# Kernel tuning notes

Measured on AMD Instinct MI355X. Metric: run time of the kernel, lower is better.

Reference implementation:

```python
import jax, jax.numpy as jnp
import numpy as np

N, L, D, H = 2, 2048, 1024, 16
Dh = D // H          # 64
HIST = 2048          # history_len
SCALE = D ** 0.5     # note: module scales by sqrt(model_dim), not sqrt(head_dim)


def setup_inputs() -> dict:
    key = jax.random.key(0)
    ks = jax.random.split(key, 10)
    f = lambda k, s, sc=1.0: jax.random.normal(k, s, dtype=jnp.float32) * sc
    i = jnp.arange(L)
    causal = i[None, :] > i[:, None]            # mask future
    old = i[None, :] <= i[:, None] - HIST       # mask beyond history window
    mask = causal | old                          # True = masked, (L, L)
    return {
        "values": f(ks[0], (N, L, D)),
        "keys": f(ks[1], (N, L, D)),
        "query": f(ks[2], (N, L, D)),
        "origin_values": f(ks[3], (N, L, D)),
        "origin_keys": f(ks[4], (N, L, D)),
        "Wv": f(ks[5], (Dh, Dh), 0.1),
        "Wk": f(ks[6], (Dh, Dh), 0.1),
        "Wq": f(ks[7], (Dh, Dh), 0.1),
        "fc_w": f(ks[8], (D, D), 0.03),
        "fc_b": jnp.zeros((D,), dtype=jnp.float32),
        "mask": mask,
    }


def reference(values, keys, query, origin_values, origin_keys, Wv, Wk, Wq, fc_w, fc_b, mask):
    # forward(..., ref_sample=True): mfpca_attention path.
    # origin_keys/values are projected exactly as the prior ref_sample=False call stored them.
    split = lambda x: x.reshape(N, L, H, Dh)
    v = split(values) @ Wv.T        # (N, L, H, Dh)  torch Linear: x @ W^T, no bias
    k = split(keys) @ Wk.T
    q = split(query) @ Wq.T
    ov = split(origin_values) @ Wv.T
    ok = split(origin_keys) @ Wk.T

    energy = jnp.einsum('nqhd,nkhd->nhqk', q, ok)       # (N, H, L, L)
    samp_energy = jnp.einsum('nlhd,nlhd->nhl', q, k)    # (N, H, L)
    eye = jnp.eye(L, dtype=bool)
    # energy.diagonal().copy_(samp_energy)
    energy = jnp.where(eye, samp_energy[:, :, None, :], energy)
    energy = jnp.where(mask, jnp.float32(-1e20), energy)
    scores = jax.nn.softmax(energy / SCALE, axis=-1)
    diag_scores = jnp.diagonal(scores, axis1=2, axis2=3)    # (N, H, L)
    scores_nodiag = jnp.where(eye, 0.0, scores)
    # NOTE: original einsum output is indexed by l (not q) -- reproduced faithfully.
    origin_attention = jnp.einsum('nhql,nlhd->nlhd', scores_nodiag, ov)
    samp_attention = jnp.einsum('nhl,nlhd->nlhd', diag_scores, v)
    attention = (samp_attention + origin_attention).reshape(N, L, D)
    return attention @ fc_w.T + fc_b
```

## Files before the change

kernel.cpp:

```cpp
#include <hip/hip_runtime.h>

#define NB 2
#define LL 2048
#define DD 1024
#define HH 16
#define NHH (NB*HH)
#define LT (LL/64)
#define KT16 (LL/16)
#define CEXP 0.0450842200277801f

typedef __bf16 bf16x8 __attribute__((ext_vector_type(8)));
typedef unsigned short u16x8 __attribute__((ext_vector_type(8)));
typedef float f32x4 __attribute__((ext_vector_type(4)));

#define MFMA16 __builtin_amdgcn_mfma_f32_16x16x32_bf16
#define EXP2 __builtin_amdgcn_exp2f
#define LOG2 __builtin_amdgcn_logf

__device__ __forceinline__ unsigned short f2bf(float f) {
    unsigned u = __float_as_uint(f);
    return (unsigned short)((u + 0x7fffu + ((u >> 16) & 1u)) >> 16);
}
__device__ __forceinline__ float bf2f(unsigned short u) {
    return __uint_as_float(((unsigned)u) << 16);
}
__device__ __forceinline__ bf16x8 ldfrag(const unsigned short* p) {
    return *reinterpret_cast<const bf16x8*>(p);
}
__device__ __forceinline__ bf16x8 cvt8v(float4 a, float4 b) {
    u16x8 u;
    u[0]=f2bf(a.x); u[1]=f2bf(a.y); u[2]=f2bf(a.z); u[3]=f2bf(a.w);
    u[4]=f2bf(b.x); u[5]=f2bf(b.y); u[6]=f2bf(b.z); u[7]=f2bf(b.w);
    return __builtin_bit_cast(bf16x8, u);
}
__device__ __forceinline__ ushort4 pack4(f32x4 d, float sc) {
    ushort4 o;
    o.x = f2bf(d[0]*sc); o.y = f2bf(d[1]*sc); o.z = f2bf(d[2]*sc); o.w = f2bf(d[3]*sc);
    return o;
}
__device__ __forceinline__ void gload16(const unsigned short* g, unsigned short* l) {
    __builtin_amdgcn_global_load_lds(
        (const __attribute__((address_space(1))) unsigned int*)g,
        (__attribute__((address_space(3))) unsigned int*)l, 16, 0, 0);
}

__global__ __launch_bounds__(256) void prep_kernel(
    const float* __restrict__ Wk, const float* __restrict__ Wq,
    const float* __restrict__ Wv, unsigned short* __restrict__ wfrag)
{
    const int t = threadIdx.x;
    const int s = blockIdx.x * 256 + t;
    const int m = s >> 9;
    const int rem = s & 511;
    const int f = rem >> 6;
    const int lane = rem & 63;
    const int n16 = lane & 15, quad = lane >> 4;
    const int mt = f >> 1, half = f & 1;
    const float* W = (m == 0) ? Wk : (m == 1) ? Wq : Wv;
    const float* p = W + (mt*16 + n16)*64 + quad*8 + half*32;
    float4 a = *reinterpret_cast<const float4*>(p);
    float4 b = *reinterpret_cast<const float4*>(p + 4);
    *reinterpret_cast<bf16x8*>(wfrag + (size_t)s * 8) = cvt8v(a, b);
}

__global__ __launch_bounds__(256) void proj_kernel(
    const float* __restrict__ values, const float* __restrict__ keys,
    const float* __restrict__ query,  const float* __restrict__ ovals,
    const float* __restrict__ okeys,  const unsigned short* __restrict__ wfrag,
    const float* __restrict__ fc_w,   unsigned short* __restrict__ fcwb,
    unsigned short* __restrict__ qb, unsigned short* __restrict__ okb,
    unsigned short* __restrict__ vb, unsigned short* __restrict__ ovb,
    float* __restrict__ ediag)
{
    const int t = threadIdx.x;
    if (blockIdx.z == 2) {
        const int id = blockIdx.y * 64 + blockIdx.x;
        const int idx = id * 1024 + t * 4;
        float4 wv = *reinterpret_cast<const float4*>(fc_w + idx);
        ushort4 o;
        o.x = f2bf(wv.x); o.y = f2bf(wv.y); o.z = f2bf(wv.z); o.w = f2bf(wv.w);
        *reinterpret_cast<ushort4*>(fcwb + idx) = o;
        return;
    }
    const int w = t >> 6;
    const int lane = t & 63;
    const int n16 = lane & 15;
    const int quad = lane >> 4;
    const int h = blockIdx.y;
    const int row = blockIdx.x * 64 + w * 16 + n16;
    const int nn = row >> 11;
    const int ll = row & 2047;
    const size_t xoff  = (size_t)row * DD + h * 64 + quad * 8;
    const size_t qbase = (((size_t)(nn * HH + h)) * LL + ll) * 64;
    const size_t vbase = (size_t)row * DD + h * 64;

    if (blockIdx.z == 0) {
        const float4* kp = reinterpret_cast<const float4*>(keys  + xoff);
        const float4* qp = reinterpret_cast<const float4*>(query + xoff);
        const float4* op = reinterpret_cast<const float4*>(okeys + xoff);
        float4 k0 = kp[0], k1 = kp[1], k2 = kp[8], k3 = kp[9];
        float4 q0 = qp[0], q1 = qp[1], q2 = qp[8], q3 = qp[9];
        float4 o0 = op[0], o1 = op[1], o2 = op[8], o3 = op[9];
        bf16x8 wk[8], wq[8];
#pragma unroll
        for (int f = 0; f < 8; ++f) {
            wk[f] = ldfrag(wfrag + (size_t)(f * 64 + lane) * 8);
            wq[f] = ldfrag(wfrag + (size_t)((8 + f) * 64 + lane) * 8);
        }
        bf16x8 xk0 = cvt8v(k0, k1), xk1 = cvt8v(k2, k3);
        bf16x8 xq0 = cvt8v(q0, q1), xq1 = cvt8v(q2, q3);
        bf16x8 xo0 = cvt8v(o0, o1), xo1 = cvt8v(o2, o3);
        f32x4 ka[4], qa[4];
#pragma unroll
        for (int mt = 0; mt < 4; ++mt) {
            f32x4 d = {0.f,0.f,0.f,0.f};
            d = MFMA16(wk[mt*2], xk0, d, 0,0,0);
            ka[mt] = MFMA16(wk[mt*2+1], xk1, d, 0,0,0);
        }
#pragma unroll
        for (int mt = 0; mt < 4; ++mt) {
            f32x4 d = {0.f,0.f,0.f,0.f};
            d = MFMA16(wq[mt*2], xq0, d, 0,0,0);
            qa[mt] = MFMA16(wq[mt*2+1], xq1, d, 0,0,0);
            *reinterpret_cast<ushort4*>(qb + qbase + mt*16 + quad*4) = pack4(qa[mt], CEXP);
        }
#pragma unroll
        for (int mt = 0; mt < 4; ++mt) {
            f32x4 d = {0.f,0.f,0.f,0.f};
            d = MFMA16(wk[mt*2], xo0, d, 0,0,0);
            d = MFMA16(wk[mt*2+1], xo1, d, 0,0,0);
            *reinterpret_cast<ushort4*>(okb + qbase + mt*16 + quad*4) = pack4(d, 1.0f);
        }
        float p = 0.f;
#pragma unroll
        for (int mt = 0; mt < 4; ++mt)
            p += qa[mt][0]*ka[mt][0] + qa[mt][1]*ka[mt][1]
               + qa[mt][2]*ka[mt][2] + qa[mt][3]*ka[mt][3];
        p += __shfl_xor(p, 16);
        p += __shfl_xor(p, 32);
        if (lane < 16)
            ediag[((size_t)(nn * HH + h)) * LL + ll] = p;
    } else {
        const float4* vp = reinterpret_cast<const float4*>(values + xoff);
        const float4* op = reinterpret_cast<const float4*>(ovals  + xoff);
        float4 v0 = vp[0], v1 = vp[1], v2 = vp[8], v3 = vp[9];
        float4 o0 = op[0], o1 = op[1], o2 = op[8], o3 = op[9];
        bf16x8 wv[8];
#pragma unroll
        for (int f = 0; f < 8; ++f)
            wv[f] = ldfrag(wfrag + (size_t)((16 + f) * 64 + lane) * 8);
        bf16x8 xv0 = cvt8v(v0, v1), xv1 = cvt8v(v2, v3);
        bf16x8 xo0 = cvt8v(o0, o1), xo1 = cvt8v(o2, o3);
#pragma unroll
        for (int mt = 0; mt < 4; ++mt) {
            f32x4 d = {0.f,0.f,0.f,0.f};
            d = MFMA16(wv[mt*2], xv0, d, 0,0,0);
            d = MFMA16(wv[mt*2+1], xv1, d, 0,0,0);
            *reinterpret_cast<ushort4*>(vb + vbase + mt*16 + quad*4) = pack4(d, 1.0f);
        }
#pragma unroll
        for (int mt = 0; mt < 4; ++mt) {
            f32x4 d = {0.f,0.f,0.f,0.f};
            d = MFMA16(wv[mt*2], xo0, d, 0,0,0);
            d = MFMA16(wv[mt*2+1], xo1, d, 0,0,0);
            *reinterpret_cast<ushort4*>(ovb + vbase + mt*16 + quad*4) = pack4(d, 1.0f);
        }
    }
}

__global__ __launch_bounds__(256) void zrow_part(
    const unsigned short* __restrict__ qb, const unsigned short* __restrict__ okb,
    float* __restrict__ Zbuf)
{
    __shared__ unsigned short slds[2][64 * 64];

    const int bid = blockIdx.x;
    const int nh = bid & 31;
    const int qt = 31 - (bid >> 5);
    const int t = threadIdx.x;
    const int w = t >> 6;
    const int lane = t & 63;
    const int n = lane & 15;
    const int quad = lane >> 4;
    const size_t base = (size_t)nh * (LL * 64);
    const size_t nhL = (size_t)nh * LL;

    const unsigned short* bp = qb + base + (size_t)(qt*64 + w*16 + n) * 64 + quad * 8;
    const bf16x8 bq0 = ldfrag(bp);
    const bf16x8 bq1 = ldfrag(bp + 32);

    const int srow = t >> 3;
    const int schunk = (t & 7) ^ (srow & 7);
    const int soff = srow * 64 + schunk * 8;
    const int nst = qt + 1;

    {
        const unsigned short* s0 = okb + base + soff;
        gload16(s0, &slds[0][t * 8]);
        gload16(s0 + 32 * 64, &slds[0][2048 + t * 8]);
    }
    __syncthreads();

    const int rs0 = (quad ^ (n & 7)) * 8;
    const int rs1 = ((quad + 4) ^ (n & 7)) * 8;

    float zacc = 0.f;
    int buf = 0;
    for (int si = 0; si < nst; ++si) {
        if (si + 1 < nst) {
            const unsigned short* s0 = okb + base + (size_t)((si + 1) * 64) * 64 + soff;
            gload16(s0, &slds[buf ^ 1][t * 8]);
            gload16(s0 + 32 * 64, &slds[buf ^ 1][2048 + t * 8]);
        }
        const unsigned short* S = &slds[buf][0];
        const bool dstrip = (si == qt);
#pragma unroll
        for (int sub = 0; sub < 4; ++sub) {
            if (dstrip && sub > w) continue;
            const int row = sub * 16 + n;
            const bf16x8 a0 = ldfrag(S + row * 64 + rs0);
            const bf16x8 a1 = ldfrag(S + row * 64 + rs1);
            f32x4 d = {0.f, 0.f, 0.f, 0.f};
            d = MFMA16(a0, bq0, d, 0, 0, 0);
            d = MFMA16(a1, bq1, d, 0, 0, 0);
            if (dstrip && sub == w) {
#pragma unroll
                for (int r = 0; r < 4; ++r)
                    if (quad * 4 + r < n) zacc += EXP2(d[r]);
            } else {
#pragma unroll
                for (int r = 0; r < 4; ++r) zacc += EXP2(d[r]);
            }
        }
        __syncthreads();
        buf ^= 1;
    }

    zacc += __shfl_down(zacc, 32);
    zacc += __shfl_down(zacc, 16);
    if (lane < 16)
        Zbuf[nhL + qt * 64 + w * 16 + lane] = zacc;
}

__global__ __launch_bounds__(256) void colsum_part(
    const unsigned short* __restrict__ qb, const unsigned short* __restrict__ okb,
    const float* __restrict__ Zbuf, const float* __restrict__ ediag,
    float* __restrict__ colsum)
{
    __shared__ unsigned short slds[2][64 * 64];
    __shared__ __align__(16) float izlds[2][64];

    const int bid = blockIdx.x;
    const int nh = bid & 31;
    const int lt = bid >> 5;
    const int t = threadIdx.x;
    const int w = t >> 6;
    const int lane = t & 63;
    const int n = lane & 15;
    const int quad = lane >> 4;
    const size_t base = (size_t)nh * (LL * 64);
    const size_t nhL = (size_t)nh * LL;

    const unsigned short* bp = okb + base + (size_t)(lt*64 + w*16 + n) * 64 + quad * 8;
    const bf16x8 bl0 = ldfrag(bp);
    const bf16x8 bl1 = ldfrag(bp + 32);

    const int srow = t >> 3;
    const int schunk = (t & 7) ^ (srow & 7);
    const int soff = srow * 64 + schunk * 8;
    const int nst = 32 - lt;
    const int q00 = lt * 64;

    {
        const unsigned short* s0 = qb + base + (size_t)q00 * 64 + soff;
        gload16(s0, &slds[0][t * 8]);
        gload16(s0 + 32 * 64, &slds[0][2048 + t * 8]);
        if (t < 64) {
            const float z = Zbuf[nhL + q00 + t];
            const float e = ediag[nhL + q00 + t];
            izlds[0][t] = -LOG2(z + EXP2(e * CEXP));
        }
    }
    __syncthreads();

    const int rs0 = (quad ^ (n & 7)) * 8;
    const int rs1 = ((quad + 4) ^ (n & 7)) * 8;

    float cacc = 0.f;
    int buf = 0;
    for (int si = 0; si < nst; ++si) {
        if (si + 1 < nst) {
            const int qn = q00 + (si + 1) * 64;
            const unsigned short* s0 = qb + base + (size_t)qn * 64 + soff;
            gload16(s0, &slds[buf ^ 1][t * 8]);
            gload16(s0 + 32 * 64, &slds[buf ^ 1][2048 + t * 8]);
            if (t < 64) {
                const float z = Zbuf[nhL + qn + t];
                const float e = ediag[nhL + qn + t];
                izlds[buf ^ 1][t] = -LOG2(z + EXP2(e * CEXP));
            }
        }
        const unsigned short* S = &slds[buf][0];
        const bool dstrip = (si == 0);
#pragma unroll
        for (int sub = 0; sub < 4; ++sub) {
            if (dstrip && sub < w) continue;
            const int row = sub * 16 + n;
            const bf16x8 a0 = ldfrag(S + row * 64 + rs0);
            const bf16x8 a1 = ldfrag(S + row * 64 + rs1);
            const f32x4 lgv = *reinterpret_cast<const f32x4*>(
                &izlds[buf][sub * 16 + quad * 4]);
            f32x4 d = lgv;
            d = MFMA16(a0, bl0, d, 0, 0, 0);
            d = MFMA16(a1, bl1, d, 0, 0, 0);
            if (dstrip && sub == w) {
#pragma unroll
                for (int r = 0; r < 4; ++r)
                    if (quad * 4 + r > n) cacc += EXP2(d[r]);
            } else {
#pragma unroll
                for (int r = 0; r < 4; ++r) cacc += EXP2(d[r]);
            }
        }
        __syncthreads();
        buf ^= 1;
    }

    cacc += __shfl_down(cacc, 32);
    cacc += __shfl_down(cacc, 16);
    if (lane < 16)
        colsum[nhL + lt * 64 + w * 16 + lane] = cacc;
}

#define LOADA(vS, ovS, zS, eS, csS, k) do {                                \
    vS  = ldfrag(pv  + (k)*32);                                            \
    ovS = ldfrag(pov + (k)*32);                                            \
    zS  = Zbuf  [scbase + ((k)>>1)*LL];                                    \
    eS  = ediag [scbase + ((k)>>1)*LL];                                    \
    csS = colsum[scbase + ((k)>>1)*LL];                                    \
} while (0)

#define CVTWRITE(vS, ovS, zS, eS, csS, dst) do {                           \
    const float de_ = EXP2(eS * CEXP);                                     \
    const float ds_ = de_ * (1.f / (zS + de_));                            \
    u16x8 vu_ = __builtin_bit_cast(u16x8, vS);                             \
    u16x8 ou_ = __builtin_bit_cast(u16x8, ovS);                            \
    u16x8 o_;                                                              \
    _Pragma("unroll")                                                      \
    for (int i_ = 0; i_ < 8; ++i_)                                         \
        o_[i_] = f2bf(ds_ * bf2f(vu_[i_]) + csS * bf2f(ou_[i_]));          \
    *reinterpret_cast<u16x8*>(dst) = o_;                                   \
} while (0)

#define COMPUTE(Abuf, Bbuf) do {                                           \
    bf16x8 af_[4], bf_[2];                                                 \
    _Pragma("unroll")                                                      \
    for (int mt = 0; mt < 4; ++mt)                                         \
        af_[mt] = ldfrag((Abuf) + (wr*64 + mt*16 + n)*32 + quad*8);        \
    _Pragma("unroll")                                                      \
    for (int nt = 0; nt < 2; ++nt)                                         \
        bf_[nt] = ldfrag((Bbuf) + (wc*32 + nt*16 + n)*32 + quad*8);        \
    _Pragma("unroll")                                                      \
    for (int mt = 0; mt < 4; ++mt)                                         \
        _Pragma("unroll")                                                  \
        for (int nt = 0; nt < 2; ++nt)                                     \
            acc[mt][nt] = MFMA16(af_[mt], bf_[nt], acc[mt][nt], 0,0,0);    \
} while (0)

__global__ __launch_bounds__(512) void out_kernel(
    const unsigned short* __restrict__ vb, const unsigned short* __restrict__ ovb,
    const float* __restrict__ Zbuf, const float* __restrict__ ediag,
    const float* __restrict__ colsum,
    const unsigned short* __restrict__ fcwb, const float* __restrict__ fc_b,
    float* __restrict__ out)
{
    __shared__ unsigned short lds[2][2][128 * 32];

    const int bid = blockIdx.x;
    const int swz = (bid & 7) * 32 + (bid >> 3);
    const int ct = swz & 7;
    const int rt = swz >> 3;
    const int row0 = rt * 128, col0 = ct * 128;

    const int t = threadIdx.x;
    const int w = t >> 6, lane = t & 63;
    const int n = lane & 15, quad = lane >> 4;
    const int wr = w >> 2, wc = w & 3;

    const int arow = row0 + (t >> 2);
    const unsigned short* pv  = vb  + (size_t)arow * DD + (t & 3) * 8;
    const unsigned short* pov = ovb + (size_t)arow * DD + (t & 3) * 8;
    const int scbase = (arow >> 11) * (HH * LL) + (arow & 2047);
    const unsigned short* gb = fcwb + (size_t)(col0 + (t >> 2)) * DD + (t & 3) * 8;
    unsigned short* la0 = &lds[0][0][t * 8];
    unsigned short* lb0 = &lds[0][1][t * 8];
    unsigned short* la1 = &lds[1][0][t * 8];
    unsigned short* lb1 = &lds[1][1][t * 8];
    const unsigned short* A0 = &lds[0][0][0];
    const unsigned short* B0 = &lds[0][1][0];
    const unsigned short* A1 = &lds[1][0][0];
    const unsigned short* B1 = &lds[1][1][0];

    f32x4 acc[4][2];
#pragma unroll
    for (int mt = 0; mt < 4; ++mt)
#pragma unroll
        for (int nt = 0; nt < 2; ++nt) acc[mt][nt] = (f32x4){0.f, 0.f, 0.f, 0.f};

    bf16x8 vP, ovP, vQ, ovQ; float zP, eP, csP, zQ, eQ, csQ;
    LOADA(vP, ovP, zP, eP, csP, 0);
    LOADA(vQ, ovQ, zQ, eQ, csQ, 1);
    gload16(gb, lb0);
    CVTWRITE(vP, ovP, zP, eP, csP, la0);
    __syncthreads();

    for (int kt = 0; kt < 32; kt += 2) {
        gload16(gb + (kt + 1) * 32, lb1);
        if (kt + 2 < 32) LOADA(vP, ovP, zP, eP, csP, kt + 2);
        COMPUTE(A0, B0);
        CVTWRITE(vQ, ovQ, zQ, eQ, csQ, la1);
        __syncthreads();
        if (kt + 2 < 32) {
            gload16(gb + (kt + 2) * 32, lb0);
            if (kt + 3 < 32) LOADA(vQ, ovQ, zQ, eQ, csQ, kt + 3);
        }
        COMPUTE(A1, B1);
        if (kt + 2 < 32) CVTWRITE(vP, ovP, zP, eP, csP, la0);
        __syncthreads();
    }

#pragma unroll
    for (int nt = 0; nt < 2; ++nt) {
        const int col = col0 + wc * 32 + nt * 16 + n;
        const float bias = fc_b[col];
#pragma unroll
        for (int mt = 0; mt < 4; ++mt)
#pragma unroll
            for (int r = 0; r < 4; ++r)
                out[(size_t)(row0 + wr * 64 + mt * 16 + quad * 4 + r) * DD + col]
                    = acc[mt][nt][r] + bias;
    }
}

extern "C" void kernel_launch(void* const* d_in, const int* in_sizes, int n_in,
                              void* d_out, int out_size, void* d_ws, size_t ws_size,
                              hipStream_t stream) {
    const float* values = (const float*)d_in[0];
    const float* keys   = (const float*)d_in[1];
    const float* query  = (const float*)d_in[2];
    const float* ovals  = (const float*)d_in[3];
    const float* okeys  = (const float*)d_in[4];
    const float* Wv     = (const float*)d_in[5];
    const float* Wk     = (const float*)d_in[6];
    const float* Wq     = (const float*)d_in[7];
    const float* fc_w   = (const float*)d_in[8];
    const float* fc_b   = (const float*)d_in[9];
    float* out = (float*)d_out;

    float* ws      = (float*)d_ws;
    float* ediag   = ws;
    float* Zbuf    = ediag + 65536;
    float* colsum  = Zbuf + 65536;
    unsigned short* qb   = (unsigned short*)(colsum + 65536);
    unsigned short* okb  = qb   + 4194304;
    unsigned short* vb   = okb  + 4194304;
    unsigned short* ovb  = vb   + 4194304;
    unsigned short* fcwb = ovb  + 4194304;
    unsigned short* wfrag = fcwb + 1048576;

    prep_kernel<<<dim3(6), 256, 0, stream>>>(Wk, Wq, Wv, wfrag);
    proj_kernel<<<dim3(64, 16, 3), 256, 0, stream>>>(
        values, keys, query, ovals, okeys, wfrag, fc_w, fcwb,
        qb, okb, vb, ovb, ediag);
    zrow_part<<<dim3(1024), 256, 0, stream>>>(qb, okb, Zbuf);
    colsum_part<<<dim3(1024), 256, 0, stream>>>(qb, okb, Zbuf, ediag, colsum);
    out_kernel<<<dim3(256), 512, 0, stream>>>(vb, ovb, Zbuf, ediag, colsum, fcwb, fc_b, out);
}
```

Before: 222.5 us.

## Fold Wq·Wk into query projection and Wv into fc weight

```diff
diff --git a/kernel.cpp b/kernel.cpp
--- a/kernel.cpp
+++ b/kernel.cpp
@@ -44,44 +44,75 @@
         (__attribute__((address_space(3))) unsigned int*)l, 16, 0, 0);
 }
 
-__global__ __launch_bounds__(256) void prep_kernel(
-    const float* __restrict__ Wk, const float* __restrict__ Wq,
-    const float* __restrict__ Wv, unsigned short* __restrict__ wfrag)
-{
-    const int t = threadIdx.x;
-    const int s = blockIdx.x * 256 + t;
-    const int m = s >> 9;
-    const int rem = s & 511;
-    const int f = rem >> 6;
-    const int lane = rem & 63;
-    const int n16 = lane & 15, quad = lane >> 4;
+__global__ __launch_bounds__(256) void prepM_kernel(
+    const float* __restrict__ Wq, const float* __restrict__ Wk,
+    unsigned short* __restrict__ wfrag)
+{
+    __shared__ float WqL[64 * 68];
+    __shared__ float WkL[64 * 68];
+    const int t = threadIdx.x;
+#pragma unroll
+    for (int j = 0; j < 4; ++j) {
+        const int p = t * 16 + j * 4;
+        const int r = p >> 6, c = p & 63;
+        *reinterpret_cast<float4*>(&WqL[r * 68 + c]) =
+            *reinterpret_cast<const float4*>(Wq + p);
+        *reinterpret_cast<float4*>(&WkL[r * 68 + c]) =
+            *reinterpret_cast<const float4*>(Wk + p);
+    }
+    __syncthreads();
+    const int s = blockIdx.x * 32 + (t >> 3);
+    const int e = t & 7;
+    const int f = s >> 6, lane = s & 63;
     const int mt = f >> 1, half = f & 1;
-    const float* W = (m == 0) ? Wk : (m == 1) ? Wq : Wv;
-    const float* p = W + (mt*16 + n16)*64 + quad*8 + half*32;
-    float4 a = *reinterpret_cast<const float4*>(p);
-    float4 b = *reinterpret_cast<const float4*>(p + 4);
-    *reinterpret_cast<bf16x8*>(wfrag + (size_t)s * 8) = cvt8v(a, b);
+    const int o = mt * 16 + (lane & 15);
+    const int k = (lane >> 4) * 8 + half * 32 + e;
+    float acc = 0.f;
+#pragma unroll 8
+    for (int i = 0; i < 64; ++i)
+        acc += WqL[i * 68 + k] * WkL[i * 68 + o];
+    wfrag[(size_t)s * 8 + e] = f2bf(acc);
+}
+
+__global__ __launch_bounds__(256) void prep2_kernel(
+    const float* __restrict__ fc_w, const float* __restrict__ Wv,
+    unsigned short* __restrict__ fcwb)
+{
+    __shared__ float wvL[64 * 64];
+    __shared__ float fcL[16 * 68];
+    const int j = blockIdx.x;
+    const int t = threadIdx.x;
+#pragma unroll
+    for (int q = 0; q < 4; ++q)
+        reinterpret_cast<float4*>(wvL)[t * 4 + q] =
+            reinterpret_cast<const float4*>(Wv)[t * 4 + q];
+    {
+        const int p = t * 4;
+        const float4 v = *reinterpret_cast<const float4*>(fc_w + (size_t)j * DD + p);
+        *reinterpret_cast<float4*>(&fcL[(p >> 6) * 68 + (p & 63)]) = v;
+    }
+    __syncthreads();
+    const int h = t >> 4, db = (t & 15) * 4;
+    float a0 = 0.f, a1 = 0.f, a2 = 0.f, a3 = 0.f;
+#pragma unroll 8
+    for (int i = 0; i < 64; ++i) {
+        const float fv = fcL[h * 68 + i];
+        const float4 wv4 = *reinterpret_cast<const float4*>(&wvL[i * 64 + db]);
+        a0 += fv * wv4.x; a1 += fv * wv4.y; a2 += fv * wv4.z; a3 += fv * wv4.w;
+    }
+    ushort4 o;
+    o.x = f2bf(a0); o.y = f2bf(a1); o.z = f2bf(a2); o.w = f2bf(a3);
+    *reinterpret_cast<ushort4*>(fcwb + (size_t)j * DD + h * 64 + db) = o;
 }
 
 __global__ __launch_bounds__(256) void proj_kernel(
-    const float* __restrict__ values, const float* __restrict__ keys,
-    const float* __restrict__ query,  const float* __restrict__ ovals,
-    const float* __restrict__ okeys,  const unsigned short* __restrict__ wfrag,
-    const float* __restrict__ fc_w,   unsigned short* __restrict__ fcwb,
+    const float* __restrict__ query, const float* __restrict__ keys,
+    const float* __restrict__ okeys, const unsigned short* __restrict__ wfrag,
     unsigned short* __restrict__ qb, unsigned short* __restrict__ okb,
-    unsigned short* __restrict__ vb, unsigned short* __restrict__ ovb,
     float* __restrict__ ediag)
 {
-    const int t = threadIdx.x;
-    if (blockIdx.z == 2) {
-        const int id = blockIdx.y * 64 + blockIdx.x;
-        const int idx = id * 1024 + t * 4;
-        float4 wv = *reinterpret_cast<const float4*>(fc_w + idx);
-        ushort4 o;
-        o.x = f2bf(wv.x); o.y = f2bf(wv.y); o.z = f2bf(wv.z); o.w = f2bf(wv.w);
-        *reinterpret_cast<ushort4*>(fcwb + idx) = o;
-        return;
-    }
+    __shared__ float eb[4][16][68];
+    const int t = threadIdx.x;
     const int w = t >> 6;
     const int lane = t & 63;
     const int n16 = lane & 15;
@@ -92,80 +123,49 @@
     const int ll = row & 2047;
     const size_t xoff  = (size_t)row * DD + h * 64 + quad * 8;
     const size_t qbase = (((size_t)(nn * HH + h)) * LL + ll) * 64;
-    const size_t vbase = (size_t)row * DD + h * 64;
-
-    if (blockIdx.z == 0) {
-        const float4* kp = reinterpret_cast<const float4*>(keys  + xoff);
-        const float4* qp = reinterpret_cast<const float4*>(query + xoff);
-        const float4* op = reinterpret_cast<const float4*>(okeys + xoff);
-        float4 k0 = kp[0], k1 = kp[1], k2 = kp[8], k3 = kp[9];
-        float4 q0 = qp[0], q1 = qp[1], q2 = qp[8], q3 = qp[9];
-        float4 o0 = op[0], o1 = op[1], o2 = op[8], o3 = op[9];
-        bf16x8 wk[8], wq[8];
-#pragma unroll
-        for (int f = 0; f < 8; ++f) {
-            wk[f] = ldfrag(wfrag + (size_t)(f * 64 + lane) * 8);
-            wq[f] = ldfrag(wfrag + (size_t)((8 + f) * 64 + lane) * 8);
-        }
-        bf16x8 xk0 = cvt8v(k0, k1), xk1 = cvt8v(k2, k3);
-        bf16x8 xq0 = cvt8v(q0, q1), xq1 = cvt8v(q2, q3);
-        bf16x8 xo0 = cvt8v(o0, o1), xo1 = cvt8v(o2, o3);
-        f32x4 ka[4], qa[4];
-#pragma unroll
-        for (int mt = 0; mt < 4; ++mt) {
-            f32x4 d = {0.f,0.f,0.f,0.f};
-            d = MFMA16(wk[mt*2], xk0, d, 0,0,0);
-            ka[mt] = MFMA16(wk[mt*2+1], xk1, d, 0,0,0);
-        }
-#pragma unroll
-        for (int mt = 0; mt < 4; ++mt) {
-            f32x4 d = {0.f,0.f,0.f,0.f};
-            d = MFMA16(wq[mt*2], xq0, d, 0,0,0);
-            qa[mt] = MFMA16(wq[mt*2+1], xq1, d, 0,0,0);
-            *reinterpret_cast<ushort4*>(qb + qbase + mt*16 + quad*4) = pack4(qa[mt], CEXP);
-        }
-#pragma unroll
-        for (int mt = 0; mt < 4; ++mt) {
-            f32x4 d = {0.f,0.f,0.f,0.f};
-            d = MFMA16(wk[mt*2], xo0, d, 0,0,0);
-            d = MFMA16(wk[mt*2+1], xo1, d, 0,0,0);
-            *reinterpret_cast<ushort4*>(okb + qbase + mt*16 + quad*4) = pack4(d, 1.0f);
-        }
-        float p = 0.f;
-#pragma unroll
-        for (int mt = 0; mt < 4; ++mt)
-            p += qa[mt][0]*ka[mt][0] + qa[mt][1]*ka[mt][1]
-               + qa[mt][2]*ka[mt][2] + qa[mt][3]*ka[mt][3];
-        p += __shfl_xor(p, 16);
-        p += __shfl_xor(p, 32);
-        if (lane < 16)
-            ediag[((size_t)(nn * HH + h)) * LL + ll] = p;
-    } else {
-        const float4* vp = reinterpret_cast<const float4*>(values + xoff);
-        const float4* op = reinterpret_cast<const float4*>(ovals  + xoff);
-        float4 v0 = vp[0], v1 = vp[1], v2 = vp[8], v3 = vp[9];
-        float4 o0 = op[0], o1 = op[1], o2 = op[8], o3 = op[9];
-        bf16x8 wv[8];
-#pragma unroll
-        for (int f = 0; f < 8; ++f)
-            wv[f] = ldfrag(wfrag + (size_t)((16 + f) * 64 + lane) * 8);
-        bf16x8 xv0 = cvt8v(v0, v1), xv1 = cvt8v(v2, v3);
-        bf16x8 xo0 = cvt8v(o0, o1), xo1 = cvt8v(o2, o3);
-#pragma unroll
-        for (int mt = 0; mt < 4; ++mt) {
-            f32x4 d = {0.f,0.f,0.f,0.f};
-            d = MFMA16(wv[mt*2], xv0, d, 0,0,0);
-            d = MFMA16(wv[mt*2+1], xv1, d, 0,0,0);
-            *reinterpret_cast<ushort4*>(vb + vbase + mt*16 + quad*4) = pack4(d, 1.0f);
-        }
-#pragma unroll
-        for (int mt = 0; mt < 4; ++mt) {
-            f32x4 d = {0.f,0.f,0.f,0.f};
-            d = MFMA16(wv[mt*2], xo0, d, 0,0,0);
-            d = MFMA16(wv[mt*2+1], xo1, d, 0,0,0);
-            *reinterpret_cast<ushort4*>(ovb + vbase + mt*16 + quad*4) = pack4(d, 1.0f);
-        }
-    }
+
+    const float4* kp = reinterpret_cast<const float4*>(keys  + xoff);
+    const float4* qp = reinterpret_cast<const float4*>(query + xoff);
+    const float4* op = reinterpret_cast<const float4*>(okeys + xoff);
+    float4 k0 = kp[0], k1 = kp[1], k2 = kp[8], k3 = kp[9];
+    float4 q0 = qp[0], q1 = qp[1], q2 = qp[8], q3 = qp[9];
+    float4 o0 = op[0], o1 = op[1], o2 = op[8], o3 = op[9];
+    bf16x8 wm[8];
+#pragma unroll
+    for (int f = 0; f < 8; ++f)
+        wm[f] = ldfrag(wfrag + (size_t)(f * 64 + lane) * 8);
+
+    bf16x8 xo0 = cvt8v(o0, o1), xo1 = cvt8v(o2, o3);
+    *reinterpret_cast<bf16x8*>(okb + qbase + quad * 8)      = xo0;
+    *reinterpret_cast<bf16x8*>(okb + qbase + 32 + quad * 8) = xo1;
+
+    bf16x8 xq0 = cvt8v(q0, q1), xq1 = cvt8v(q2, q3);
+    f32x4 qa[4];
+#pragma unroll
+    for (int mt = 0; mt < 4; ++mt) {
+        f32x4 d = {0.f,0.f,0.f,0.f};
+        d = MFMA16(wm[mt*2], xq0, d, 0,0,0);
+        qa[mt] = MFMA16(wm[mt*2+1], xq1, d, 0,0,0);
+        *reinterpret_cast<ushort4*>(qb + qbase + mt*16 + quad*4) = pack4(qa[mt], CEXP);
+    }
+
+#pragma unroll
+    for (int mt = 0; mt < 4; ++mt)
+        *reinterpret_cast<f32x4*>(&eb[w][n16][mt*16 + quad*4]) = qa[mt];
+    __syncthreads();
+    const float* rp = eb[w][n16];
+    const float4 a0 = *reinterpret_cast<const float4*>(&rp[quad*8]);
+    const float4 a1 = *reinterpret_cast<const float4*>(&rp[quad*8 + 4]);
+    const float4 a2 = *reinterpret_cast<const float4*>(&rp[32 + quad*8]);
+    const float4 a3 = *reinterpret_cast<const float4*>(&rp[32 + quad*8 + 4]);
+    float p = a0.x*k0.x + a0.y*k0.y + a0.z*k0.z + a0.w*k0.w
+            + a1.x*k1.x + a1.y*k1.y + a1.z*k1.z + a1.w*k1.w
+            + a2.x*k2.x + a2.y*k2.y + a2.z*k2.z + a2.w*k2.w
+            + a3.x*k3.x + a3.y*k3.y + a3.z*k3.z + a3.w*k3.w;
+    p += __shfl_xor(p, 16);
+    p += __shfl_xor(p, 32);
+    if (lane < 16)
+        ediag[((size_t)(nn * HH + h)) * LL + ll] = p;
 }
 
 __global__ __launch_bounds__(256) void zrow_part(
@@ -332,23 +332,28 @@
         colsum[nhL + lt * 64 + w * 16 + lane] = cacc;
 }
 
-#define LOADA(vS, ovS, zS, eS, csS, k) do {                                \
-    vS  = ldfrag(pv  + (k)*32);                                            \
-    ovS = ldfrag(pov + (k)*32);                                            \
+#define LOADA(v0S, v1S, o0S, o1S, zS, eS, csS, k) do {                     \
+    v0S = *reinterpret_cast<const float4*>(pv  + (k)*32);                  \
+    v1S = *reinterpret_cast<const float4*>(pv  + (k)*32 + 4);              \
+    o0S = *reinterpret_cast<const float4*>(pov + (k)*32);                  \
+    o1S = *reinterpret_cast<const float4*>(pov + (k)*32 + 4);              \
     zS  = Zbuf  [scbase + ((k)>>1)*LL];                                    \
     eS  = ediag [scbase + ((k)>>1)*LL];                                    \
     csS = colsum[scbase + ((k)>>1)*LL];                                    \
 } while (0)
 
-#define CVTWRITE(vS, ovS, zS, eS, csS, dst) do {                           \
+#define CVTWRITE(v0S, v1S, o0S, o1S, zS, eS, csS, dst) do {                \
     const float de_ = EXP2(eS * CEXP);                                     \
     const float ds_ = de_ * (1.f / (zS + de_));                            \
-    u16x8 vu_ = __builtin_bit_cast(u16x8, vS);                             \
-    u16x8 ou_ = __builtin_bit_cast(u16x8, ovS);                            \
     u16x8 o_;                                                              \
-    _Pragma("unroll")                                                      \
-    for (int i_ = 0; i_ < 8; ++i_)                                         \
-        o_[i_] = f2bf(ds_ * bf2f(vu_[i_]) + csS * bf2f(ou_[i_]));          \
+    o_[0] = f2bf(ds_*v0S.x + csS*o0S.x);                                   \
+    o_[1] = f2bf(ds_*v0S.y + csS*o0S.y);                                   \
+    o_[2] = f2bf(ds_*v0S.z + csS*o0S.z);                                   \
+    o_[3] = f2bf(ds_*v0S.w + csS*o0S.w);                                   \
+    o_[4] = f2bf(ds_*v1S.x + csS*o1S.x);                                   \
+    o_[5] = f2bf(ds_*v1S.y + csS*o1S.y);                                   \
+    o_[6] = f2bf(ds_*v1S.z + csS*o1S.z);                                   \
+    o_[7] = f2bf(ds_*v1S.w + csS*o1S.w);                                   \
     *reinterpret_cast<u16x8*>(dst) = o_;                                   \
 } while (0)
 
@@ -368,7 +373,7 @@
 } while (0)
 
 __global__ __launch_bounds__(512) void out_kernel(
-    const unsigned short* __restrict__ vb, const unsigned short* __restrict__ ovb,
+    const float* __restrict__ values, const float* __restrict__ ovals,
     const float* __restrict__ Zbuf, const float* __restrict__ ediag,
     const float* __restrict__ colsum,
     const unsigned short* __restrict__ fcwb, const float* __restrict__ fc_b,
@@ -388,8 +393,8 @@
     const int wr = w >> 2, wc = w & 3;
 
     const int arow = row0 + (t >> 2);
-    const unsigned short* pv  = vb  + (size_t)arow * DD + (t & 3) * 8;
-    const unsigned short* pov = ovb + (size_t)arow * DD + (t & 3) * 8;
+    const float* pv  = values + (size_t)arow * DD + (t & 3) * 8;
+    const float* pov = ovals  + (size_t)arow * DD + (t & 3) * 8;
     const int scbase = (arow >> 11) * (HH * LL) + (arow & 2047);
     const unsigned short* gb = fcwb + (size_t)(col0 + (t >> 2)) * DD + (t & 3) * 8;
     unsigned short* la0 = &lds[0][0][t * 8];
@@ -407,25 +412,26 @@
 #pragma unroll
         for (int nt = 0; nt < 2; ++nt) acc[mt][nt] = (f32x4){0.f, 0.f, 0.f, 0.f};
 
-    bf16x8 vP, ovP, vQ, ovQ; float zP, eP, csP, zQ, eQ, csQ;
-    LOADA(vP, ovP, zP, eP, csP, 0);
-    LOADA(vQ, ovQ, zQ, eQ, csQ, 1);
+    float4 vP0, vP1, oP0, oP1, vQ0, vQ1, oQ0, oQ1;
+    float zP, eP, csP, zQ, eQ, csQ;
+    LOADA(vP0, vP1, oP0, oP1, zP, eP, csP, 0);
+    LOADA(vQ0, vQ1, oQ0, oQ1, zQ, eQ, csQ, 1);
     gload16(gb, lb0);
-    CVTWRITE(vP, ovP, zP, eP, csP, la0);
+    CVTWRITE(vP0, vP1, oP0, oP1, zP, eP, csP, la0);
     __syncthreads();
 
     for (int kt = 0; kt < 32; kt += 2) {
         gload16(gb + (kt + 1) * 32, lb1);
-        if (kt + 2 < 32) LOADA(vP, ovP, zP, eP, csP, kt + 2);
+        if (kt + 2 < 32) LOADA(vP0, vP1, oP0, oP1, zP, eP, csP, kt + 2);
         COMPUTE(A0, B0);
-        CVTWRITE(vQ, ovQ, zQ, eQ, csQ, la1);
+        CVTWRITE(vQ0, vQ1, oQ0, oQ1, zQ, eQ, csQ, la1);
         __syncthreads();
         if (kt + 2 < 32) {
             gload16(gb + (kt + 2) * 32, lb0);
-            if (kt + 3 < 32) LOADA(vQ, ovQ, zQ, eQ, csQ, kt + 3);
+            if (kt + 3 < 32) LOADA(vQ0, vQ1, oQ0, oQ1, zQ, eQ, csQ, kt + 3);
         }
         COMPUTE(A1, B1);
-        if (kt + 2 < 32) CVTWRITE(vP, ovP, zP, eP, csP, la0);
+        if (kt + 2 < 32) CVTWRITE(vP0, vP1, oP0, oP1, zP, eP, csP, la0);
         __syncthreads();
     }
 
@@ -463,16 +469,15 @@
     float* colsum  = Zbuf + 65536;
     unsigned short* qb   = (unsigned short*)(colsum + 65536);
     unsigned short* okb  = qb   + 4194304;
-    unsigned short* vb   = okb  + 4194304;
-    unsigned short* ovb  = vb   + 4194304;
-    unsigned short* fcwb = ovb  + 4194304;
+    unsigned short* fcwb = okb  + 4194304;
     unsigned short* wfrag = fcwb + 1048576;
 
-    prep_kernel<<<dim3(6), 256, 0, stream>>>(Wk, Wq, Wv, wfrag);
-    proj_kernel<<<dim3(64, 16, 3), 256, 0, stream>>>(
-        values, keys, query, ovals, okeys, wfrag, fc_w, fcwb,
-        qb, okb, vb, ovb, ediag);
+    prepM_kernel<<<dim3(16), 256, 0, stream>>>(Wq, Wk, wfrag);
+    proj_kernel<<<dim3(64, 16), 256, 0, stream>>>(
+        query, keys, okeys, wfrag, qb, okb, ediag);
+    prep2_kernel<<<dim3(1024), 256, 0, stream>>>(fc_w, Wv, fcwb);
     zrow_part<<<dim3(1024), 256, 0, stream>>>(qb, okb, Zbuf);
     colsum_part<<<dim3(1024), 256, 0, stream>>>(qb, okb, Zbuf, ediag, colsum);
-    out_kernel<<<dim3(256), 512, 0, stream>>>(vb, ovb, Zbuf, ediag, colsum, fcwb, fc_b, out);
-}
+    out_kernel<<<dim3(256), 512, 0, stream>>>(
+        values, ovals, Zbuf, ediag, colsum, fcwb, fc_b, out);
+}
```

New measurement: 231.0 us. 1.04x slower.
